# Kernel tuning notes

Hardware: AMD Instinct MI355X
Metric: run time of the kernel (lower is better)

Reference implementation:

```python
import jax, jax.numpy as jnp
import numpy as np

N_POINTS = 2_000_000
N_BATCH = 8


def cart2polar(xyz):
    rho = jnp.sqrt(xyz[:, 0] ** 2 + xyz[:, 1] ** 2)
    phi = jnp.arctan2(xyz[:, 1], xyz[:, 0])
    return jnp.stack((rho, phi, xyz[:, 2]), axis=1)


def setup_inputs() -> dict:
    key = jax.random.key(0)
    k1, k2, k3, k4 = jax.random.split(key, 4)
    xy = jax.random.uniform(k1, (N_POINTS, 2), minval=-50.0, maxval=50.0)
    z = jax.random.uniform(k2, (N_POINTS, 1), minval=-4.0, maxval=2.0)
    inten = jax.random.uniform(k3, (N_POINTS, 1))
    points = jnp.concatenate([xy, z, inten], axis=1)  # [N, 4]
    batch_idx = jnp.sort(jax.random.randint(k4, (N_POINTS,), 0, N_BATCH)).astype(jnp.int32)
    coors_range_xyz = jnp.array([[0.0, 50.0], [-np.pi, np.pi], [-4.0, 2.0]], dtype=jnp.float32)
    spatial_shape = np.array([480, 360, 32])  # static
    scale_list = np.array([2, 4, 1])          # module appends 1; static
    return dict(points=points, batch_idx=batch_idx,
                coors_range_xyz=coors_range_xyz,
                spatial_shape=spatial_shape, scale_list=scale_list)


def _unique_rows(bxyz, dims):
    # Encode [b, gx, gy, gz] rows into a single int32 key (max 8*480*360*32 ~ 44M).
    key = ((bxyz[:, 0] * dims[0] + bxyz[:, 1]) * dims[1] + bxyz[:, 2]) * dims[2] + bxyz[:, 3]
    order = jnp.argsort(key)
    sk = key[order]
    flags = jnp.concatenate([jnp.ones((1,), bool), sk[1:] != sk[:-1]])
    rank = jnp.cumsum(flags.astype(jnp.int32)) - 1          # unique-id per sorted row
    inv = jnp.zeros_like(rank).at[order].set(rank)           # inverse map, like torch.unique
    # first occurrence of each unique row (all rows with same rank are identical)
    unq = jnp.zeros_like(bxyz).at[rank].set(bxyz[order])     # padded to [N, 4]
    num_unique = rank[-1] + 1
    return unq, inv, num_unique


def reference(points, batch_idx, coors_range_xyz, spatial_shape, scale_list):
    pc = points[:, :3]
    xyz_pol = cart2polar(pc)
    lo = coors_range_xyz[:, 0]
    hi = coors_range_xyz[:, 1]
    crop = hi - lo
    ss_np = np.asarray(spatial_shape)
    outs = []
    for scale in [int(s) for s in np.asarray(scale_list)]:
        cells = jnp.asarray(np.ceil(ss_np / scale) - 1.0, dtype=xyz_pol.dtype)
        grid = jnp.floor((jnp.clip(xyz_pol, lo, hi) - lo) / crop * cells).astype(jnp.int32)
        bxyz = jnp.concatenate([batch_idx[:, None].astype(jnp.int32), grid], axis=1)  # [N,4]
        dims = np.ceil(ss_np / scale).astype(np.int64)
        unq, inv, num = _unique_rows(bxyz, dims)
        # reorder unique coords as [b, z, y, x], cast int32 (torch: unq[:, [0,3,2,1]])
        coors = jnp.concatenate([unq[:, 0:1], unq[:, 3:4], unq[:, 2:3], unq[:, 1:2]], axis=1).astype(jnp.int32)
        outs.extend([bxyz, inv, coors, num])
    return tuple(outs)
```

## Files before the change

kernel.cpp:

```cpp
#include <hip/hip_runtime.h>
#include <cstdint>

#define DI __device__ __forceinline__

constexpr int NPTS       = 2000000;
constexpr int STRIDE_OUT = 18000001;
constexpr int OFF_INV    = 8000000;
constexpr int OFF_COORS  = 10000000;
constexpr int OFF_NUM    = 18000000;

constexpr int R2W  = 172800;
constexpr int R4W  = 21600;
constexpr int R1W  = 1382400;
constexpr int RW0  = 0;
constexpr int RW1  = R2W;
constexpr int RW2  = R2W + R4W;
constexpr int WTOT = R2W + R4W + R1W;
constexpr int NB1  = (WTOT + 1023) / 1024;
constexpr int J2   = 8;
constexpr int P1   = 6;
constexpr int J1   = 4;
constexpr int S1W  = 28800;
constexpr int S1BITS = S1W * 32;

constexpr int NBLK_INV   = (NPTS + 255) / 256;
constexpr int NBLK_COORS = (WTOT + 255) / 256;
constexpr int NBLK_TAIL  = (3 * NPTS + 255) / 256;

DI float fmul_s(float a, float b){ float r; asm("v_mul_f32 %0, %1, %2" : "=v"(r) : "v"(a), "v"(b)); return r; }
DI float fadd_s(float a, float b){ float r; asm("v_add_f32 %0, %1, %2" : "=v"(r) : "v"(a), "v"(b)); return r; }

DI void compute_keys(float x, float y, float z, int b, int (&key)[3]) {
  const float PI_F     = 3.14159265358979323846f;
  const float TWO_PI_F = 6.28318530717958647692f;
  float rho = sqrtf(fadd_s(fmul_s(x, x), fmul_s(y, y)));
  float phi = atan2f(y, x);
  float tr = (fminf(fmaxf(rho, 0.0f), 50.0f) - 0.0f) / 50.0f;
  float tp = (fminf(fmaxf(phi, -PI_F), PI_F) + PI_F) / TWO_PI_F;
  float tz = (fminf(fmaxf(z, -4.0f), 2.0f) + 4.0f) / 6.0f;
  constexpr float C0[3] = {239.f, 119.f, 479.f};
  constexpr float C1[3] = {179.f,  89.f, 359.f};
  constexpr float C2[3] = { 15.f,   7.f,  31.f};
  constexpr int   D0[3] = {240, 120, 480};
  constexpr int   D1[3] = {180,  90, 360};
  constexpr int   D2[3] = { 16,   8,  32};
  #pragma unroll
  for (int s = 0; s < 3; ++s) {
    int a0 = (int)floorf(tr * C0[s]);
    int a1 = (int)floorf(tp * C1[s]);
    int a2 = (int)floorf(tz * C2[s]);
    key[s] = ((b * D0[s] + a0) * D1[s] + a1) * D2[s] + a2;
  }
}

DI int lower_bound(const int* __restrict__ a, int n, int v) {
  int lo = 0, hi = n;
  while (lo < hi) { int m = (lo + hi) >> 1; if (a[m] < v) lo = m + 1; else hi = m; }
  return lo;
}

__global__ __launch_bounds__(256) void pass_keys(const float4* __restrict__ pts,
                                                 const int* __restrict__ batch, int n,
                                                 int* __restrict__ keys) {
  int i = blockIdx.x * 256 + threadIdx.x;
  if (i >= n) return;
  float4 p = pts[i];
  int key[3];
  compute_keys(p.x, p.y, p.z, batch[i], key);
  keys[i] = key[0]; keys[n + i] = key[1]; keys[2 * n + i] = key[2];
}

__global__ __launch_bounds__(1024) void hist_all(const int* __restrict__ batch,
                                                 const int* __restrict__ keys, int n,
                                                 uint32_t* __restrict__ rep2s,
                                                 uint32_t* __restrict__ rep4s,
                                                 uint32_t* __restrict__ rep1s) {
  alignas(16) __shared__ uint32_t bmA[S1W];
  alignas(16) __shared__ uint32_t bmB[2700];
  int t = threadIdx.x;
  if ((int)blockIdx.x < 64) {
    int bv = blockIdx.x >> 3, j = blockIdx.x & 7;
    for (int w = t * 4; w < 21600; w += 4096) *reinterpret_cast<uint4*>(bmA + w) = make_uint4(0,0,0,0);
    for (int w = t; w < 2700; w += 1024) bmB[w] = 0;
    __syncthreads();
    int lo = lower_bound(batch, n, bv);
    int hi = lower_bound(batch, n, bv + 1);
    int sz = hi - lo;
    int s = lo + (int)((long long)sz * j / J2);
    int e = lo + (int)((long long)sz * (j + 1) / J2);
    const int* k0 = keys;
    const int* k1 = keys + n;
    for (int i = s + t; i < e; i += 1024) {
      int ink2 = k0[i] - bv * 691200;
      int ink4 = k1[i] - bv * 86400;
      atomicOr(&bmA[ink2 >> 5], 1u << (ink2 & 31));
      atomicOr(&bmB[ink4 >> 5], 1u << (ink4 & 31));
    }
    __syncthreads();
    uint32_t* d2 = rep2s + (size_t)j * R2W + bv * 21600;
    uint32_t* d4 = rep4s + (size_t)j * R4W + bv * 2700;
    for (int w = t * 4; w < 21600; w += 4096) *reinterpret_cast<uint4*>(d2 + w) = *reinterpret_cast<uint4*>(bmA + w);
    for (int w = t * 4; w < 2700; w += 4096) *reinterpret_cast<uint4*>(d4 + w) = *reinterpret_cast<uint4*>(bmB + w);
  } else {
    int idx = blockIdx.x - 64;
    int j = idx / 48;
    int slice = idx - j * 48;
    int bv = slice / 6, r = slice - bv * 6;
    for (int w = t * 4; w < S1W; w += 4096) *reinterpret_cast<uint4*>(bmA + w) = make_uint4(0,0,0,0);
    __syncthreads();
    int lo = lower_bound(batch, n, bv);
    int hi = lower_bound(batch, n, bv + 1);
    int sz = hi - lo;
    int s = lo + (int)((long long)sz * j / J1);
    int e = lo + (int)((long long)sz * (j + 1) / J1);
    const int* k2 = keys + 2 * n;
    int base = bv * 5529600 + r * S1BITS;
    for (int i = s + t; i < e; i += 1024) {
      int rel = k2[i] - base;
      if ((unsigned)rel < (unsigned)S1BITS) atomicOr(&bmA[rel >> 5], 1u << (rel & 31));
    }
    __syncthreads();
    uint32_t* d = rep1s + (size_t)j * R1W + (size_t)slice * S1W;
    for (int w = t * 4; w < S1W; w += 4096) *reinterpret_cast<uint4*>(d + w) = *reinterpret_cast<uint4*>(bmA + w);
  }
}

DI uint4 merged_words(int base, const uint32_t* __restrict__ rep2s,
                      const uint32_t* __restrict__ rep4s,
                      const uint32_t* __restrict__ rep1s) {
  uint4 acc = make_uint4(0, 0, 0, 0);
  if (base < RW1) {
    #pragma unroll
    for (int c = 0; c < J2; ++c) {
      uint4 w = *reinterpret_cast<const uint4*>(rep2s + (size_t)c * R2W + base);
      acc.x |= w.x; acc.y |= w.y; acc.z |= w.z; acc.w |= w.w;
    }
  } else if (base < RW2) {
    int l = base - RW1;
    #pragma unroll
    for (int c = 0; c < J2; ++c) {
      uint4 w = *reinterpret_cast<const uint4*>(rep4s + (size_t)c * R4W + l);
      acc.x |= w.x; acc.y |= w.y; acc.z |= w.z; acc.w |= w.w;
    }
  } else {
    int l = base - RW2;
    #pragma unroll
    for (int c = 0; c < J1; ++c) {
      uint4 w = *reinterpret_cast<const uint4*>(rep1s + (size_t)c * R1W + l);
      acc.x |= w.x; acc.y |= w.y; acc.z |= w.z; acc.w |= w.w;
    }
  }
  return acc;
}

__global__ __launch_bounds__(256) void scanA(const uint32_t* __restrict__ rep2s,
                                             const uint32_t* __restrict__ rep4s,
                                             const uint32_t* __restrict__ rep1s,
                                             uint32_t* __restrict__ bits,
                                             uint32_t* __restrict__ blockSums) {
  __shared__ uint32_t lds[256];
  int t = threadIdx.x;
  int base = blockIdx.x * 1024 + t * 4;
  uint32_t s = 0;
  if (base < WTOT) {
    uint4 m = merged_words(base, rep2s, rep4s, rep1s);
    *reinterpret_cast<uint4*>(bits + base) = m;
    s = __popc(m.x) + __popc(m.y) + __popc(m.z) + __popc(m.w);
  }
  lds[t] = s; __syncthreads();
  for (int off = 128; off > 0; off >>= 1) { if (t < off) lds[t] += lds[t + off]; __syncthreads(); }
  if (t == 0) blockSums[blockIdx.x] = lds[0];
}

__global__ __launch_bounds__(256) void scanC(const uint32_t* __restrict__ bits,
                                             const uint32_t* __restrict__ blockSums,
                                             uint2* __restrict__ pairs) {
  __shared__ uint32_t lds[256];
  int t = threadIdx.x;
  uint32_t bs = 0;
  for (int k = t; k < (int)blockIdx.x; k += 256) bs += blockSums[k];
  lds[t] = bs; __syncthreads();
  for (int off = 128; off > 0; off >>= 1) { if (t < off) lds[t] += lds[t + off]; __syncthreads(); }
  uint32_t blockBase = lds[0];
  __syncthreads();
  int base = blockIdx.x * 1024 + t * 4;
  uint32_t b[4] = {0,0,0,0}; uint32_t c[4]; uint32_t sum = 0;
  if (base < WTOT) {
    uint4 w = *reinterpret_cast<const uint4*>(bits + base);
    b[0] = w.x; b[1] = w.y; b[2] = w.z; b[3] = w.w;
  }
  #pragma unroll
  for (int k = 0; k < 4; ++k) { c[k] = __popc(b[k]); sum += c[k]; }
  lds[t] = sum; __syncthreads();
  for (int off = 1; off < 256; off <<= 1) {
    uint32_t x = (t >= off) ? lds[t - off] : 0u; __syncthreads();
    lds[t] += x; __syncthreads();
  }
  uint32_t excl = lds[t] - sum + blockBase;
  if (base < WTOT) {
    #pragma unroll
    for (int k = 0; k < 4; ++k) { pairs[base + k] = make_uint2(b[k], excl); excl += c[k]; }
  }
}

template <int S>
DI int4 decode_key(int key) {
  constexpr int D0[3] = {240, 120, 480};
  constexpr int D1[3] = {180,  90, 360};
  constexpr int D2[3] = { 16,   8,  32};
  int a2 = key & (D2[S] - 1);
  int r  = key / D2[S];
  int q  = r / D1[S];
  int a1 = r - q * D1[S];
  int b  = q / D0[S];
  int a0 = q - b * D0[S];
  return make_int4(b, a0, a1, a2);
}

template <int S>
DI void coors_word(int wi_local, uint32_t bits, uint32_t rank, int* __restrict__ coors) {
  int keybase = wi_local * 32;
  while (bits) {
    int j = __builtin_ctz(bits);
    bits &= bits - 1;
    int4 d = decode_key<S>(keybase + j);
    *reinterpret_cast<int4*>(coors + (size_t)rank * 4) = make_int4(d.x, d.w, d.z, d.y);
    ++rank;
  }
}

__global__ __launch_bounds__(256) void epilogue(int n, const uint2* __restrict__ pairs,
                                                const int* __restrict__ keys,
                                                int* __restrict__ out) {
  int b = blockIdx.x;
  int t = threadIdx.x;
  if (b < NBLK_INV) {
    int i = b * 256 + t;
    if (i >= n) return;
    int key[3] = { keys[i], keys[n + i], keys[2 * n + i] };
    constexpr int RW[3] = {RW0, RW1, RW2};
    *reinterpret_cast<int4*>(out + 0 * STRIDE_OUT + i * 4) = decode_key<0>(key[0]);
    *reinterpret_cast<int4*>(out + 1 * STRIDE_OUT + i * 4) = decode_key<1>(key[1]);
    *reinterpret_cast<int4*>(out + 2 * STRIDE_OUT + i * 4) = decode_key<2>(key[2]);
    #pragma unroll
    for (int s = 0; s < 3; ++s) {
      uint2 pr = pairs[RW[s] + (key[s] >> 5)];
      uint32_t base = pr.y - ((s == 0) ? 0u : pairs[RW[s]].y);
      int rank = (int)(base + __popc(pr.x & ((1u << (key[s] & 31)) - 1u)));
      out[s * STRIDE_OUT + OFF_INV + i] = rank;
    }
  } else if (b < NBLK_INV + NBLK_COORS) {
    int wi = (b - NBLK_INV) * 256 + t;
    if (wi >= WTOT) return;
    uint2 pr = pairs[wi];
    if (!pr.x) return;
    if (wi < RW1)      coors_word<0>(wi,       pr.x, pr.y,                 out + 0 * STRIDE_OUT + OFF_COORS);
    else if (wi < RW2) coors_word<1>(wi - RW1, pr.x, pr.y - pairs[RW1].y,  out + 1 * STRIDE_OUT + OFF_COORS);
    else               coors_word<2>(wi - RW2, pr.x, pr.y - pairs[RW2].y,  out + 2 * STRIDE_OUT + OFF_COORS);
  } else {
    int idx = (b - NBLK_INV - NBLK_COORS) * 256 + t;
    if (idx >= 3 * n) return;
    int s = 0, i = idx;
    if (i >= 2 * n)  { s = 2; i -= 2 * n; }
    else if (i >= n) { s = 1; i -= n; }
    uint2 last = pairs[WTOT - 1];
    uint32_t total = last.y + (uint32_t)__popc(last.x);
    uint32_t lo = (s == 0) ? 0u : pairs[(s == 1) ? RW1 : RW2].y;
    uint32_t hi = (s == 0) ? pairs[RW1].y : (s == 1) ? pairs[RW2].y : total;
    uint32_t num = hi - lo;
    if (i == 0) out[s * STRIDE_OUT + OFF_NUM] = (int)num;
    if ((uint32_t)i >= num)
      *reinterpret_cast<int4*>(out + s * STRIDE_OUT + OFF_COORS + (size_t)i * 4) = make_int4(0, 0, 0, 0);
  }
}

extern "C" void kernel_launch(void* const* d_in, const int* in_sizes, int n_in,
                              void* d_out, int out_size, void* d_ws, size_t ws_size,
                              hipStream_t stream) {
  const float4* pts   = (const float4*)d_in[0];
  const int*    batch = (const int*)d_in[1];
  int n = in_sizes[1];
  int* out = (int*)d_out;

  uint32_t* rep2s     = (uint32_t*)d_ws;
  uint32_t* rep4s     = rep2s + (size_t)J2 * R2W;
  uint32_t* rep1s     = rep4s + (size_t)J2 * R4W;
  uint32_t* bits      = rep1s + (size_t)J1 * R1W;
  uint2*    pairs     = (uint2*)(bits + WTOT);
  uint32_t* blockSums = (uint32_t*)(pairs + WTOT);
  int*      keys      = (int*)(blockSums + NB1 + 16);

  int nblk = (n + 255) / 256;
  pass_keys<<<nblk, 256, 0, stream>>>(pts, batch, n, keys);
  hist_all<<<256, 1024, 0, stream>>>(batch, keys, n, rep2s, rep4s, rep1s);
  scanA<<<NB1, 256, 0, stream>>>(rep2s, rep4s, rep1s, bits, blockSums);
  scanC<<<NB1, 256, 0, stream>>>(bits, blockSums, pairs);
  epilogue<<<NBLK_INV + NBLK_COORS + NBLK_TAIL, 256, 0, stream>>>(n, pairs, keys, out);
}
```

Measured before the change: 348.2 us.

## Record batch boundaries in key pass and remap block indices across XCDs

The key-computation kernel now writes the start offset of each batch into a small workspace array. The histogram kernel reads those offsets directly, replacing two binary searches over the 2M-entry batch array in every block. Block-to-work mapping in the histogram and epilogue kernels is also permuted (batch on the low bits, strided interleave) so consecutive block IDs scatter across chiplets and neighbouring work shares cache. The boundary write loop assumes sorted batch indices and adds a small divergent store in boundary threads.

```diff
diff --git a/kernel.cpp b/kernel.cpp
--- a/kernel.cpp
+++ b/kernel.cpp
@@ -24,6 +24,8 @@
 constexpr int S1BITS = S1W * 32;
 
 constexpr int NBLK_INV   = (NPTS + 255) / 256;
+constexpr int NBLK_INV8  = ((NBLK_INV + 7) / 8) * 8;
+constexpr int INV_QUOT   = NBLK_INV8 / 8;
 constexpr int NBLK_COORS = (WTOT + 255) / 256;
 constexpr int NBLK_TAIL  = (3 * NPTS + 255) / 256;
 
@@ -53,24 +55,27 @@
   }
 }
 
-DI int lower_bound(const int* __restrict__ a, int n, int v) {
-  int lo = 0, hi = n;
-  while (lo < hi) { int m = (lo + hi) >> 1; if (a[m] < v) lo = m + 1; else hi = m; }
-  return lo;
-}
-
 __global__ __launch_bounds__(256) void pass_keys(const float4* __restrict__ pts,
                                                  const int* __restrict__ batch, int n,
-                                                 int* __restrict__ keys) {
+                                                 int* __restrict__ keys,
+                                                 int* __restrict__ bstart) {
   int i = blockIdx.x * 256 + threadIdx.x;
   if (i >= n) return;
   float4 p = pts[i];
+  int bi = batch[i];
   int key[3];
-  compute_keys(p.x, p.y, p.z, batch[i], key);
+  compute_keys(p.x, p.y, p.z, bi, key);
   keys[i] = key[0]; keys[n + i] = key[1]; keys[2 * n + i] = key[2];
-}
-
-__global__ __launch_bounds__(1024) void hist_all(const int* __restrict__ batch,
+  if (i == 0) {
+    #pragma unroll 1
+    for (int k = 0; k <= bi; ++k) bstart[k] = 0;
+  }
+  int bnext = (i + 1 < n) ? batch[i + 1] : 8;
+  #pragma unroll 1
+  for (int k = bi + 1; k <= bnext; ++k) bstart[k] = i + 1;
+}
+
+__global__ __launch_bounds__(1024) void hist_all(const int* __restrict__ bstart,
                                                  const int* __restrict__ keys, int n,
                                                  uint32_t* __restrict__ rep2s,
                                                  uint32_t* __restrict__ rep4s,
@@ -78,13 +83,14 @@
   alignas(16) __shared__ uint32_t bmA[S1W];
   alignas(16) __shared__ uint32_t bmB[2700];
   int t = threadIdx.x;
-  if ((int)blockIdx.x < 64) {
-    int bv = blockIdx.x >> 3, j = blockIdx.x & 7;
+  int pb = blockIdx.x;
+  if (pb < 64) {
+    int bv = pb & 7, j = pb >> 3;
     for (int w = t * 4; w < 21600; w += 4096) *reinterpret_cast<uint4*>(bmA + w) = make_uint4(0,0,0,0);
     for (int w = t; w < 2700; w += 1024) bmB[w] = 0;
     __syncthreads();
-    int lo = lower_bound(batch, n, bv);
-    int hi = lower_bound(batch, n, bv + 1);
+    int lo = bstart[bv];
+    int hi = bstart[bv + 1];
     int sz = hi - lo;
     int s = lo + (int)((long long)sz * j / J2);
     int e = lo + (int)((long long)sz * (j + 1) / J2);
@@ -102,14 +108,14 @@
     for (int w = t * 4; w < 21600; w += 4096) *reinterpret_cast<uint4*>(d2 + w) = *reinterpret_cast<uint4*>(bmA + w);
     for (int w = t * 4; w < 2700; w += 4096) *reinterpret_cast<uint4*>(d4 + w) = *reinterpret_cast<uint4*>(bmB + w);
   } else {
-    int idx = blockIdx.x - 64;
-    int j = idx / 48;
-    int slice = idx - j * 48;
-    int bv = slice / 6, r = slice - bv * 6;
+    int bv = pb & 7;
+    int id = (pb - 64) >> 3;
+    int j = id / 6, r = id - j * 6;
+    int slice = bv * 6 + r;
     for (int w = t * 4; w < S1W; w += 4096) *reinterpret_cast<uint4*>(bmA + w) = make_uint4(0,0,0,0);
     __syncthreads();
-    int lo = lower_bound(batch, n, bv);
-    int hi = lower_bound(batch, n, bv + 1);
+    int lo = bstart[bv];
+    int hi = bstart[bv + 1];
     int sz = hi - lo;
     int s = lo + (int)((long long)sz * j / J1);
     int e = lo + (int)((long long)sz * (j + 1) / J1);
@@ -234,8 +240,10 @@
                                                 int* __restrict__ out) {
   int b = blockIdx.x;
   int t = threadIdx.x;
-  if (b < NBLK_INV) {
-    int i = b * 256 + t;
+  if (b < NBLK_INV8) {
+    int l = (b & 7) * INV_QUOT + (b >> 3);
+    if (l >= NBLK_INV) return;
+    int i = l * 256 + t;
     if (i >= n) return;
     int key[3] = { keys[i], keys[n + i], keys[2 * n + i] };
     constexpr int RW[3] = {RW0, RW1, RW2};
@@ -249,8 +257,8 @@
       int rank = (int)(base + __popc(pr.x & ((1u << (key[s] & 31)) - 1u)));
       out[s * STRIDE_OUT + OFF_INV + i] = rank;
     }
-  } else if (b < NBLK_INV + NBLK_COORS) {
-    int wi = (b - NBLK_INV) * 256 + t;
+  } else if (b < NBLK_INV8 + NBLK_COORS) {
+    int wi = (b - NBLK_INV8) * 256 + t;
     if (wi >= WTOT) return;
     uint2 pr = pairs[wi];
     if (!pr.x) return;
@@ -258,7 +266,7 @@
     else if (wi < RW2) coors_word<1>(wi - RW1, pr.x, pr.y - pairs[RW1].y,  out + 1 * STRIDE_OUT + OFF_COORS);
     else               coors_word<2>(wi - RW2, pr.x, pr.y - pairs[RW2].y,  out + 2 * STRIDE_OUT + OFF_COORS);
   } else {
-    int idx = (b - NBLK_INV - NBLK_COORS) * 256 + t;
+    int idx = (b - NBLK_INV8 - NBLK_COORS) * 256 + t;
     if (idx >= 3 * n) return;
     int s = 0, i = idx;
     if (i >= 2 * n)  { s = 2; i -= 2 * n; }
@@ -288,12 +296,13 @@
   uint32_t* bits      = rep1s + (size_t)J1 * R1W;
   uint2*    pairs     = (uint2*)(bits + WTOT);
   uint32_t* blockSums = (uint32_t*)(pairs + WTOT);
-  int*      keys      = (int*)(blockSums + NB1 + 16);
+  int*      bstart    = (int*)(blockSums + NB1);
+  int*      keys      = (int*)(bstart + 16);
 
   int nblk = (n + 255) / 256;
-  pass_keys<<<nblk, 256, 0, stream>>>(pts, batch, n, keys);
-  hist_all<<<256, 1024, 0, stream>>>(batch, keys, n, rep2s, rep4s, rep1s);
+  pass_keys<<<nblk, 256, 0, stream>>>(pts, batch, n, keys, bstart);
+  hist_all<<<256, 1024, 0, stream>>>(bstart, keys, n, rep2s, rep4s, rep1s);
   scanA<<<NB1, 256, 0, stream>>>(rep2s, rep4s, rep1s, bits, blockSums);
   scanC<<<NB1, 256, 0, stream>>>(bits, blockSums, pairs);
-  epilogue<<<NBLK_INV + NBLK_COORS + NBLK_TAIL, 256, 0, stream>>>(n, pairs, keys, out);
-}
+  epilogue<<<NBLK_INV8 + NBLK_COORS + NBLK_TAIL, 256, 0, stream>>>(n, pairs, keys, out);
+}
```

Result: faster. 328.2 us (-5.7%).
